# Optimization experiments

Hardware: AMD Instinct MI355X
Metric: run time of the kernel (lower is better)

## Reference

```python
import jax, jax.numpy as jnp
import numpy as np

# module config (matches init_kwargs)
SLICE_W, SLICE_H = 32, 32
STRIDE, WIDTH_INIT = 8, 8
EMBED_DIM = 512
B, H, W = 64, 32, 4096
PAD = (SLICE_W - WIDTH_INIT) // 2  # 12, width padding with constant value 1.0


def setup_inputs() -> dict:
    key = jax.random.key(0)
    k1, k2, k3, k4, k5 = jax.random.split(key, 5)
    u = lambda k, s: jax.random.uniform(k, s, jnp.float32, -0.08, 0.08)
    return {
        "images": jax.random.normal(k1, (B, 1, H, W), jnp.float32),
        "conv_w": u(k2, (1, 1, 3, 3)),          # Conv2d(1,1,3x3) weight (OIHW)
        "conv_b": u(k3, (1,)),
        "lin_w": u(k4, (SLICE_W * SLICE_H, EMBED_DIM)),  # bridge Linear, stored [in,out]
        "lin_b": u(k5, (EMBED_DIM,)),
    }


def reference(images, conv_w, conv_b, lin_w, lin_b):
    b = images.shape[0]
    # pad width with constant 1 (F.pad(..., 'constant', 1))
    padded = jnp.pad(images, ((0, 0), (0, 0), (0, 0), (PAD, PAD)), constant_values=1.0)
    # vectorized replacement of the python loop over stride positions
    starts = np.arange(0, W - 1, STRIDE)               # [S] static
    S = starts.shape[0]                                # 512
    idx = starts[:, None] + np.arange(SLICE_W)[None, :]  # [S, slice_w]
    sl = padded[:, :, :, idx]                          # [B,1,H,S,slice_w]
    sl = jnp.transpose(sl, (0, 3, 1, 2, 4))            # [B,S,1,H,slice_w]
    x = sl.reshape(b * S, 1, H, SLICE_W)               # pixels
    # embedder: Conv2d(1,1,k=3,pad=1) + ReLU
    y = jax.lax.conv_general_dilated(x, conv_w, (1, 1), ((1, 1), (1, 1)))
    y = jax.nn.relu(y + conv_b[None, :, None, None])
    # bridge: Linear(slice_w*slice_h -> embed_dim)
    flat = y.reshape(b * S, H * SLICE_W)
    out = flat @ lin_w + lin_b
    return out.reshape(b, S, EMBED_DIM)
```

## Files before the change

kernel.cpp:

```cpp
#include <hip/hip_runtime.h>
#include <cstdint>
#include <cstddef>

typedef unsigned short u16;
typedef unsigned int   u32;
typedef __attribute__((ext_vector_type(4))) float  f32x4;
typedef __attribute__((ext_vector_type(2))) u32    u32x2;
typedef __attribute__((ext_vector_type(8))) __bf16 bf16x8;

#define PSW   1056
#define ASTR  72
#define CFW   4128
#define RPAD  4128

#define WS_BT  0u
#define WS_CF  1048576u
#define WS_AB  (1048576u + 16908288u)
#define WS_NEED (1048576u + 16908288u + 4194304u)

static __device__ __forceinline__ float b2f(u32 u) {
  union { u32 i; float f; } c; c.i = u << 16; return c.f;
}
static __device__ __forceinline__ u16 f2b(float f) {
  union { float f; u32 i; } c; c.f = f;
  return (u16)((c.i + 0x7FFFu + ((c.i >> 16) & 1u)) >> 16);
}

static __device__ __forceinline__ void gl_lds16(const void* g, void* l) {
  __builtin_amdgcn_global_load_lds(
      (__attribute__((address_space(1))) unsigned int*)(void*)g,
      (__attribute__((address_space(3))) unsigned int*)l, 16, 0, 0);
}
static __device__ __forceinline__ void gl_lds4(const void* g, void* l) {
  __builtin_amdgcn_global_load_lds(
      (__attribute__((address_space(1))) unsigned int*)(void*)g,
      (__attribute__((address_space(3))) unsigned int*)l, 4, 0, 0);
}

__global__ __launch_bounds__(256) void transpose_w(const float* __restrict__ lw,
                                                   u16* __restrict__ bt) {
  __shared__ u16 tile[64][65];
  const int t  = threadIdx.x;
  const int c  = t & 63, r0 = t >> 6;
  const int n0 = blockIdx.x * 64;
  const int k0 = blockIdx.y * 64;
#pragma unroll
  for (int rr = 0; rr < 16; ++rr) {
    const int r = r0 * 16 + rr;
    tile[r][c] = f2b(lw[(size_t)(k0 + r) * 512 + n0 + c]);
  }
  __syncthreads();
#pragma unroll
  for (int rr = 0; rr < 16; ++rr) {
    const int r = r0 * 16 + rr;
    bt[(size_t)(n0 + r) * 1024 + k0 + c] = tile[c][r];
  }
}

__global__ __launch_bounds__(256) void prep(
    const float* __restrict__ img, const float* __restrict__ cw,
    const float* __restrict__ cb, u16* __restrict__ cf, u32* __restrict__ ab,
    const float* __restrict__ lw, u16* __restrict__ bt)
{
  __shared__ __align__(16) float R[3][RPAD];
  const int t = threadIdx.x;

  if (blockIdx.y == 32) {
    u16* tile = (u16*)&R[0][0];
    const int c = t & 63, r0 = t >> 6;
#pragma unroll
    for (int q = 0; q < 2; ++q) {
      const int T  = blockIdx.x * 2 + q;
      const int n0 = (T & 7) << 6, k0 = (T >> 3) << 6;
      __syncthreads();
#pragma unroll
      for (int rr = 0; rr < 16; ++rr) {
        const int r = r0 * 16 + rr;
        tile[r * 65 + c] = f2b(lw[(size_t)(k0 + r) * 512 + n0 + c]);
      }
      __syncthreads();
#pragma unroll
      for (int rr = 0; rr < 16; ++rr) {
        const int r = r0 * 16 + rr;
        bt[(size_t)(n0 + r) * 1024 + k0 + c] = tile[c * 65 + r];
      }
    }
    return;
  }

  const int b = blockIdx.x, h = blockIdx.y;
  const float* imgb = img + (size_t)b * 32 * 4096;
#pragma unroll
  for (int r = 0; r < 3; ++r) {
    const int hh = h - 1 + r;
    const int live = (hh >= 0 && hh <= 31);
    const float live1 = live ? 1.0f : 0.0f;
    const float* row = imgb + (ptrdiff_t)hh * 4096;
    for (int k = t; k < 1024; k += 256) {
      f32x4 v = (f32x4)0.0f;
      if (live) v = *(const f32x4*)(row + (k << 2));
      *(f32x4*)(&R[r][16 + (k << 2)]) = v;
    }
    if (t < 12)      R[r][4 + t]    = live1;
    else if (t < 24) R[r][4100 + t] = live1;
    else if (t < 28) R[r][4100 + t] = 0.0f;
    else if (t < 32) R[r][t - 28]   = 0.0f;
  }
  __syncthreads();
  float w[9];
#pragma unroll
  for (int q = 0; q < 9; ++q) w[q] = cw[q];
  const float bias = cb[0];
  u16* dst = cf + (size_t)(b * 32 + h) * CFW;
  if (t == 0) *(uint4*)(dst + 4120) = make_uint4(0u, 0u, 0u, 0u);

  for (int c4 = t; c4 < 1030; c4 += 256) {
    float wf[3][12];
#pragma unroll
    for (int r = 0; r < 3; ++r) {
      const f32x4* Rr = (const f32x4*)&R[r][0];
      *(f32x4*)&wf[r][0] = Rr[c4];
      *(f32x4*)&wf[r][4] = Rr[c4 + 1];
      *(f32x4*)&wf[r][8] = Rr[c4 + 2];
    }
    float o[4];
#pragma unroll
    for (int j = 0; j < 4; ++j) o[j] = bias;
#pragma unroll
    for (int r = 0; r < 3; ++r) {
      const float w0 = w[r * 3], w1 = w[r * 3 + 1], w2 = w[r * 3 + 2];
#pragma unroll
      for (int j = 0; j < 4; ++j)
        o[j] += w0 * wf[r][j + 3] + w1 * wf[r][j + 4] + w2 * wf[r][j + 5];
    }
    u32x2 pk;
    pk.x = (u32)f2b(fmaxf(o[0], 0.f)) | ((u32)f2b(fmaxf(o[1], 0.f)) << 16);
    pk.y = (u32)f2b(fmaxf(o[2], 0.f)) | ((u32)f2b(fmaxf(o[3], 0.f)) << 16);
    *(u32x2*)(dst + (c4 << 2)) = pk;
  }

  u32* abrow = ab + (size_t)(b * 32 + h) * 512;
#pragma unroll
  for (int ss = 0; ss < 2; ++ss) {
    const int s  = t + (ss << 8);
    const int X0 = (s << 3) + 4;
    float o0 = bias, o1 = bias;
#pragma unroll
    for (int r = 0; r < 3; ++r) {
      o0 += w[r * 3 + 1] * R[r][X0]      + w[r * 3 + 2] * R[r][X0 + 1];
      o1 += w[r * 3 + 0] * R[r][X0 + 30] + w[r * 3 + 1] * R[r][X0 + 31];
    }
    abrow[s] = (u32)f2b(fmaxf(o0, 0.f)) | ((u32)f2b(fmaxf(o1, 0.f)) << 16);
  }
}

__global__ __launch_bounds__(256) void gemm_k(
    const u16* __restrict__ cf, const u32* __restrict__ ab,
    const u16* __restrict__ bt, const float* __restrict__ lb,
    float* __restrict__ out)
{
  __shared__ __align__(16) char sm[4224 + 1024 + 16384];
  u16* Ps   = (u16*)sm;
  u32* Ab32 = (u32*)(sm + 4224);
  u16* Bs   = (u16*)(sm + 5248);
  float* Cs = (float*)sm;

  const int t  = threadIdx.x;
  const int orig = blockIdx.y * 4 + blockIdx.x;
  const int wg   = ((orig & 7) << 7) + (orig >> 3);
  const int nt = wg & 3, mt = wg >> 2;
  const int b  = mt >> 2, s0 = (mt & 3) << 7, n0 = nt << 7;
  const int w  = t >> 6, i = t & 63;
  const int wr = w >> 1, wc = w & 1;
  const int lq = i >> 4, lr = i & 15;

  const int cB = (i & 7) ^ ((i >> 3) & 7);
  const u16* btp = bt + (size_t)(n0 + (w << 5) + (i >> 3)) * 1024 + (cB << 3);
  u16* BsW = Bs + (w << 11);

  const int rP  = (t >= 132) ? 1 : 0;
  const int ccP = t - 132 * rP;
  const u16* cfp  = cf + (size_t)(b * 32 + rP) * CFW + (s0 << 3) + (ccP << 3);
  const u16* cfp2 = cf + (size_t)(b * 32 + 1) * CFW + (s0 << 3) + ((124 + t) << 3);
  u16* PsW = Ps + (w << 9);

  const u32* abp = ab + (size_t)(b * 32 + (t >> 7)) * 512 + s0 + (t & 127);
  u32* AbW = Ab32 + (w << 6);

  f32x4 acc[4][4];
#pragma unroll
  for (int a = 0; a < 4; ++a)
#pragma unroll
    for (int c = 0; c < 4; ++c) acc[a][c] = (f32x4)0.0f;

  for (int kk = 0; kk < 16; ++kk) {
    __syncthreads();
    gl_lds16(btp,              BsW);
    gl_lds16(btp +  8 * 1024,  BsW + 512);
    gl_lds16(btp + 16 * 1024,  BsW + 1024);
    gl_lds16(btp + 24 * 1024,  BsW + 1536);
    gl_lds16(cfp, PsW);
    if (t < 8) gl_lds16(cfp2, Ps + 2048);
    gl_lds4(abp, AbW);
    btp += 64; cfp += 2 * CFW; cfp2 += 2 * CFW; abp += 1024;
    __syncthreads();

#pragma unroll
    for (int kc = 0; kc < 2; ++kc) {
      const int bswz = (((kc << 2) + lq) ^ (lr & 7)) << 3;
      bf16x8 af[4], bfv[4];
#pragma unroll
      for (int im = 0; im < 4; ++im) {
        const int ml = wr * 64 + im * 16 + lr;
        af[im] = __builtin_bit_cast(bf16x8,
            *(const uint4*)(Ps + kc * 1056 + ((ml + lq) << 3)));
        const u32 a32 = Ab32[kc * 128 + ml];
        union { u16 u; __bf16 h; } lo, hi;
        lo.u = (u16)(a32 & 0xffffu); hi.u = (u16)(a32 >> 16);
        if (lq == 0) af[im][0] = lo.h;
        if (lq == 3) af[im][7] = hi.h;
      }
#pragma unroll
      for (int jn = 0; jn < 4; ++jn) {
        const int n = wc * 64 + jn * 16 + lr;
        bfv[jn] = __builtin_bit_cast(bf16x8, *(const uint4*)(Bs + (n << 6) + bswz));
      }
#pragma unroll
      for (int im = 0; im < 4; ++im)
#pragma unroll
        for (int jn = 0; jn < 4; ++jn)
          acc[im][jn] = __builtin_amdgcn_mfma_f32_16x16x32_bf16(
              af[im], bfv[jn], acc[im][jn], 0, 0, 0);
    }
  }

  float lbv[4];
#pragma unroll
  for (int jn = 0; jn < 4; ++jn) lbv[jn] = lb[n0 + wc * 64 + jn * 16 + lr];

  const int erow = t >> 3, ecol = (t & 7) << 4;
  const int grow_base = (mt << 7) + ((erow >> 4) * 64) + (erow & 15);

#pragma unroll
  for (int im = 0; im < 4; ++im) {
    __syncthreads();
#pragma unroll
    for (int jn = 0; jn < 4; ++jn) {
      const int cl = wc * 64 + jn * 16 + lr;
#pragma unroll
      for (int r = 0; r < 4; ++r)
        Cs[(wr * 16 + lq * 4 + r) * 132 + cl] = acc[im][jn][r] + lbv[jn];
    }
    __syncthreads();
    const size_t grow = (size_t)(grow_base + im * 16);
    float* orow = out + grow * 512 + n0 + ecol;
    const float* crow = Cs + erow * 132 + ecol;
#pragma unroll
    for (int p = 0; p < 4; ++p)
      *(f32x4*)(orow + p * 4) = *(const f32x4*)(crow + p * 4);
  }
}

__global__ __launch_bounds__(256) void fused_fallback(
    const float* __restrict__ img, const float* __restrict__ cw,
    const float* __restrict__ cb, const u16* __restrict__ bt,
    const float* __restrict__ lb, float* __restrict__ out)
{
  __shared__ __align__(16) u16 Ps[4 * PSW];
  __shared__ __align__(16) u16 As[128 * ASTR];
  __shared__ __align__(16) u16 Bs[128 * ASTR];
  const int t = threadIdx.x, nt = blockIdx.x, mt = blockIdx.y;
  const int b = mt >> 2, s0 = (mt & 3) << 7, X0 = s0 << 3, n0 = nt << 7;
  const float* imgb = img + (size_t)b * 32 * 4096;
  float cwf[9];
#pragma unroll
  for (int q = 0; q < 9; ++q) cwf[q] = cw[q];
  const float bias = cb[0];
  const int wv = t >> 6, l = t & 63;
  const int wr = wv >> 1, wc = wv & 1, lq = l >> 4, lr = l & 15;
  const int sl = t >> 1, hsel = t & 1;
  f32x4 acc[4][4];
#pragma unroll
  for (int a = 0; a < 4; ++a)
#pragma unroll
    for (int c = 0; c < 4; ++c) acc[a][c] = (f32x4)0.0f;
  for (int kk = 0; kk < 16; ++kk) {
    const int h0 = kk << 1;
    __syncthreads();
    uint4 bsv[4];
#pragma unroll
    for (int p = 0; p < 4; ++p) {
      const int idx8 = t + (p << 8);
      const int n = idx8 >> 3, k8 = idx8 & 7;
      bsv[p] = *(const uint4*)(bt + (size_t)(n0 + n) * 1024 + (kk << 6) + (k8 << 3));
    }
    for (int idx = t; idx < 4 * PSW; idx += 256) {
      const int r = idx / PSW, xi = idx - r * PSW;
      const int h = h0 - 1 + r, x = X0 - 1 + xi;
      u16 v = 0;
      if (h >= 0 && h < 32 && x >= 0 && x < 4120)
        v = (x < 12 || x >= 4108) ? (u16)0x3F80 : f2b(imgb[h * 4096 + (x - 12)]);
      Ps[idx] = v;
    }
    __syncthreads();
    {
      const int pbase = (sl << 3);
#pragma unroll
      for (int wb = 0; wb < 32; wb += 16) {
        float o[16];
#pragma unroll
        for (int j = 0; j < 16; ++j) o[j] = bias;
#pragma unroll
        for (int dr = 0; dr < 3; ++dr) {
          const u16* p = Ps + (hsel + dr) * PSW + pbase + wb;
          const uint4 va = *(const uint4*)p;
          const uint4 vb = *(const uint4*)(p + 8);
          const u32   vc = *(const u32*)(p + 16);
          float win[18];
          win[0] = b2f(va.x & 0xffffu); win[1] = b2f(va.x >> 16);
          win[2] = b2f(va.y & 0xffffu); win[3] = b2f(va.y >> 16);
          win[4] = b2f(va.z & 0xffffu); win[5] = b2f(va.z >> 16);
          win[6] = b2f(va.w & 0xffffu); win[7] = b2f(va.w >> 16);
          win[8] = b2f(vb.x & 0xffffu); win[9] = b2f(vb.x >> 16);
          win[10] = b2f(vb.y & 0xffffu); win[11] = b2f(vb.y >> 16);
          win[12] = b2f(vb.z & 0xffffu); win[13] = b2f(vb.z >> 16);
          win[14] = b2f(vb.w & 0xffffu); win[15] = b2f(vb.w >> 16);
          win[16] = b2f(vc & 0xffffu);   win[17] = b2f(vc >> 16);
          if (wb == 0) win[0] = 0.f; else win[17] = 0.f;
          const float w0 = cwf[dr * 3], w1 = cwf[dr * 3 + 1], w2 = cwf[dr * 3 + 2];
#pragma unroll
          for (int j = 0; j < 16; ++j)
            o[j] += w0 * win[j] + w1 * win[j + 1] + w2 * win[j + 2];
        }
        u32 pk[8];
#pragma unroll
        for (int q = 0; q < 8; ++q)
          pk[q] = (u32)f2b(fmaxf(o[2 * q], 0.f)) | ((u32)f2b(fmaxf(o[2 * q + 1], 0.f)) << 16);
        uint4* dst = (uint4*)(As + sl * ASTR + (hsel << 5) + wb);
        dst[0] = make_uint4(pk[0], pk[1], pk[2], pk[3]);
        dst[1] = make_uint4(pk[4], pk[5], pk[6], pk[7]);
      }
    }
#pragma unroll
    for (int p = 0; p < 4; ++p) {
      const int idx8 = t + (p << 8);
      const int n = idx8 >> 3, k8 = idx8 & 7;
      *(uint4*)(Bs + n * ASTR + (k8 << 3)) = bsv[p];
    }
    __syncthreads();
#pragma unroll
    for (int kc = 0; kc < 2; ++kc) {
      const int ko = (kc << 5) + (lq << 3);
      bf16x8 af[4], bfv[4];
#pragma unroll
      for (int im = 0; im < 4; ++im)
        af[im] = __builtin_bit_cast(bf16x8,
            *(const uint4*)(As + (wr * 64 + im * 16 + lr) * ASTR + ko));
#pragma unroll
      for (int jn = 0; jn < 4; ++jn)
        bfv[jn] = __builtin_bit_cast(bf16x8,
            *(const uint4*)(Bs + (wc * 64 + jn * 16 + lr) * ASTR + ko));
#pragma unroll
      for (int im = 0; im < 4; ++im)
#pragma unroll
        for (int jn = 0; jn < 4; ++jn)
          acc[im][jn] = __builtin_amdgcn_mfma_f32_16x16x32_bf16(
              af[im], bfv[jn], acc[im][jn], 0, 0, 0);
    }
  }
#pragma unroll
  for (int jn = 0; jn < 4; ++jn) {
    const int col = n0 + wc * 64 + jn * 16 + lr;
    const float lbv = lb[col];
#pragma unroll
    for (int im = 0; im < 4; ++im) {
      const int row0 = (mt << 7) + wr * 64 + im * 16 + (lq << 2);
#pragma unroll
      for (int r = 0; r < 4; ++r)
        out[(size_t)(row0 + r) * 512 + col] = acc[im][jn][r] + lbv;
    }
  }
}

extern "C" void kernel_launch(void* const* d_in, const int* in_sizes, int n_in,
                              void* d_out, int out_size, void* d_ws, size_t ws_size,
                              hipStream_t stream) {
  const float* img = (const float*)d_in[0];
  const float* cw  = (const float*)d_in[1];
  const float* cb  = (const float*)d_in[2];
  const float* lw  = (const float*)d_in[3];
  const float* lb  = (const float*)d_in[4];
  float* out = (float*)d_out;

  u16* btw = (u16*)((char*)d_ws + WS_BT);

  if (ws_size >= WS_NEED) {
    u16* cfp = (u16*)((char*)d_ws + WS_CF);
    u32* abp = (u32*)((char*)d_ws + WS_AB);
    prep<<<dim3(64, 33), 256, 0, stream>>>(img, cw, cb, cfp, abp, lw, btw);
    gemm_k<<<dim3(4, 256), 256, 0, stream>>>(cfp, abp, btw, lb, out);
  } else {
    transpose_w<<<dim3(8, 16), 256, 0, stream>>>(lw, btw);
    fused_fallback<<<dim3(4, 256), 256, 0, stream>>>(img, cw, cb, btw, lb, out);
  }
}
```

Measured before the change: 165.2 us.

## Double-buffer GEMM LDS stages and remap prep block indices

Splits the GEMM k-loop into stage and compute steps over two LDS buffers, so global-to-LDS loads for the next k-slice are issued while MFMAs run on the current one. This removes one barrier per iteration and hides load latency, at the cost of roughly doubling LDS use per block, which may lower occupancy. The prep kernel also moves from a 2D grid to a linearized, XCD-interleaved block-to-(b,h) mapping. It still keeps the weight-transpose blocks at h==32.

```diff
diff --git a/kernel.cpp b/kernel.cpp
--- a/kernel.cpp
+++ b/kernel.cpp
@@ -12,6 +12,7 @@
 #define ASTR  72
 #define CFW   4128
 #define RPAD  4128
+#define BUFB  21632
 
 #define WS_BT  0u
 #define WS_CF  1048576u
@@ -65,12 +66,16 @@
   __shared__ __align__(16) float R[3][RPAD];
   const int t = threadIdx.x;
 
-  if (blockIdx.y == 32) {
+  const int hwid = blockIdx.y * 64 + blockIdx.x;
+  const int g = (hwid & 7) * 264 + (hwid >> 3);
+  const int b = g / 33, h = g - b * 33;
+
+  if (h == 32) {
     u16* tile = (u16*)&R[0][0];
     const int c = t & 63, r0 = t >> 6;
 #pragma unroll
     for (int q = 0; q < 2; ++q) {
-      const int T  = blockIdx.x * 2 + q;
+      const int T  = b * 2 + q;
       const int n0 = (T & 7) << 6, k0 = (T >> 3) << 6;
       __syncthreads();
 #pragma unroll
@@ -88,7 +93,6 @@
     return;
   }
 
-  const int b = blockIdx.x, h = blockIdx.y;
   const float* imgb = img + (size_t)b * 32 * 4096;
 #pragma unroll
   for (int r = 0; r < 3; ++r) {
@@ -159,10 +163,7 @@
     const u16* __restrict__ bt, const float* __restrict__ lb,
     float* __restrict__ out)
 {
-  __shared__ __align__(16) char sm[4224 + 1024 + 16384];
-  u16* Ps   = (u16*)sm;
-  u32* Ab32 = (u32*)(sm + 4224);
-  u16* Bs   = (u16*)(sm + 5248);
+  __shared__ __align__(16) char sm[2 * BUFB];
   float* Cs = (float*)sm;
 
   const int t  = threadIdx.x;
@@ -176,16 +177,11 @@
 
   const int cB = (i & 7) ^ ((i >> 3) & 7);
   const u16* btp = bt + (size_t)(n0 + (w << 5) + (i >> 3)) * 1024 + (cB << 3);
-  u16* BsW = Bs + (w << 11);
-
   const int rP  = (t >= 132) ? 1 : 0;
   const int ccP = t - 132 * rP;
   const u16* cfp  = cf + (size_t)(b * 32 + rP) * CFW + (s0 << 3) + (ccP << 3);
   const u16* cfp2 = cf + (size_t)(b * 32 + 1) * CFW + (s0 << 3) + ((124 + t) << 3);
-  u16* PsW = Ps + (w << 9);
-
   const u32* abp = ab + (size_t)(b * 32 + (t >> 7)) * 512 + s0 + (t & 127);
-  u32* AbW = Ab32 + (w << 6);
 
   f32x4 acc[4][4];
 #pragma unroll
@@ -193,18 +189,24 @@
 #pragma unroll
     for (int c = 0; c < 4; ++c) acc[a][c] = (f32x4)0.0f;
 
-  for (int kk = 0; kk < 16; ++kk) {
-    __syncthreads();
+  auto STAGE = [&](char* base) {
+    u16* PsB = (u16*)base;
+    u32* AbB = (u32*)(base + 4224);
+    u16* BsW = (u16*)(base + 5248) + (w << 11);
     gl_lds16(btp,              BsW);
     gl_lds16(btp +  8 * 1024,  BsW + 512);
     gl_lds16(btp + 16 * 1024,  BsW + 1024);
     gl_lds16(btp + 24 * 1024,  BsW + 1536);
-    gl_lds16(cfp, PsW);
-    if (t < 8) gl_lds16(cfp2, Ps + 2048);
-    gl_lds4(abp, AbW);
+    gl_lds16(cfp, PsB + (w << 9));
+    if (t < 8) gl_lds16(cfp2, PsB + 2048);
+    gl_lds4(abp, AbB + (w << 6));
     btp += 64; cfp += 2 * CFW; cfp2 += 2 * CFW; abp += 1024;
-    __syncthreads();
-
+  };
+
+  auto COMPUTE = [&](const char* base) {
+    const u16* PsC = (const u16*)base;
+    const u32* AbC = (const u32*)(base + 4224);
+    const u16* BsC = (const u16*)(base + 5248);
 #pragma unroll
     for (int kc = 0; kc < 2; ++kc) {
       const int bswz = (((kc << 2) + lq) ^ (lr & 7)) << 3;
@@ -213,8 +215,8 @@
       for (int im = 0; im < 4; ++im) {
         const int ml = wr * 64 + im * 16 + lr;
         af[im] = __builtin_bit_cast(bf16x8,
-            *(const uint4*)(Ps + kc * 1056 + ((ml + lq) << 3)));
-        const u32 a32 = Ab32[kc * 128 + ml];
+            *(const uint4*)(PsC + kc * 1056 + ((ml + lq) << 3)));
+        const u32 a32 = AbC[kc * 128 + ml];
         union { u16 u; __bf16 h; } lo, hi;
         lo.u = (u16)(a32 & 0xffffu); hi.u = (u16)(a32 >> 16);
         if (lq == 0) af[im][0] = lo.h;
@@ -223,7 +225,7 @@
 #pragma unroll
       for (int jn = 0; jn < 4; ++jn) {
         const int n = wc * 64 + jn * 16 + lr;
-        bfv[jn] = __builtin_bit_cast(bf16x8, *(const uint4*)(Bs + (n << 6) + bswz));
+        bfv[jn] = __builtin_bit_cast(bf16x8, *(const uint4*)(BsC + (n << 6) + bswz));
       }
 #pragma unroll
       for (int im = 0; im < 4; ++im)
@@ -232,7 +234,23 @@
           acc[im][jn] = __builtin_amdgcn_mfma_f32_16x16x32_bf16(
               af[im], bfv[jn], acc[im][jn], 0, 0, 0);
     }
-  }
+  };
+
+  STAGE(sm);
+  __syncthreads();
+#pragma unroll 1
+  for (int kk = 0; kk < 14; kk += 2) {
+    STAGE(sm + BUFB);
+    COMPUTE(sm);
+    __syncthreads();
+    STAGE(sm);
+    COMPUTE(sm + BUFB);
+    __syncthreads();
+  }
+  STAGE(sm + BUFB);
+  COMPUTE(sm);
+  __syncthreads();
+  COMPUTE(sm + BUFB);
 
   float lbv[4];
 #pragma unroll
```

After: 164.4 us. No clear change (-0.5%).

## Restructure conv prep into row-streaming blocks with async LDS ring buffer

Applied to the files above, without the earlier changes.

Replaces the per-(batch,row) prep kernel, which loaded three image rows for every output row, with blocks that each handle a half-width column chunk and eight consecutive rows. Rows are streamed into a 4-slot LDS ring with global_load_lds, so each input row is loaded once per block and the next row's load overlaps with the current row's convolution. Block size goes to 512 threads and the weight-transpose work is packed into 8 blocks. The price is more synchronisation per row, tricky boundary indexing for the split halves and edge columns, and fewer, larger blocks.

```diff
diff --git a/kernel.cpp b/kernel.cpp
--- a/kernel.cpp
+++ b/kernel.cpp
@@ -5,13 +5,14 @@
 typedef unsigned short u16;
 typedef unsigned int   u32;
 typedef __attribute__((ext_vector_type(4))) float  f32x4;
+typedef __attribute__((ext_vector_type(2))) float  f32x2;
 typedef __attribute__((ext_vector_type(2))) u32    u32x2;
 typedef __attribute__((ext_vector_type(8))) __bf16 bf16x8;
 
 #define PSW   1056
 #define ASTR  72
 #define CFW   4128
-#define RPAD  4128
+#define WIN   2080
 
 #define WS_BT  0u
 #define WS_CF  1048576u
@@ -57,100 +58,139 @@
   }
 }
 
-__global__ __launch_bounds__(256) void prep(
+__global__ __launch_bounds__(512) void prep2(
     const float* __restrict__ img, const float* __restrict__ cw,
     const float* __restrict__ cb, u16* __restrict__ cf, u32* __restrict__ ab,
     const float* __restrict__ lw, u16* __restrict__ bt)
 {
-  __shared__ __align__(16) float R[3][RPAD];
-  const int t = threadIdx.x;
-
-  if (blockIdx.y == 32) {
-    u16* tile = (u16*)&R[0][0];
+  __shared__ __align__(16) float RING[4 * WIN];
+  const int t  = threadIdx.x;
+  const int id = blockIdx.x;
+
+  if (id >= 512) {
+    u16* tile = (u16*)&RING[0];
     const int c = t & 63, r0 = t >> 6;
-#pragma unroll
-    for (int q = 0; q < 2; ++q) {
-      const int T  = blockIdx.x * 2 + q;
+    for (int q = 0; q < 16; ++q) {
+      const int T  = (id - 512) * 16 + q;
       const int n0 = (T & 7) << 6, k0 = (T >> 3) << 6;
       __syncthreads();
 #pragma unroll
-      for (int rr = 0; rr < 16; ++rr) {
-        const int r = r0 * 16 + rr;
+      for (int rr = 0; rr < 8; ++rr) {
+        const int r = r0 * 8 + rr;
         tile[r * 65 + c] = f2b(lw[(size_t)(k0 + r) * 512 + n0 + c]);
       }
       __syncthreads();
 #pragma unroll
-      for (int rr = 0; rr < 16; ++rr) {
-        const int r = r0 * 16 + rr;
+      for (int rr = 0; rr < 8; ++rr) {
+        const int r = r0 * 8 + rr;
         bt[(size_t)(n0 + r) * 1024 + k0 + c] = tile[c * 65 + r];
       }
     }
     return;
   }
 
-  const int b = blockIdx.x, h = blockIdx.y;
+  const int b  = id >> 3, sub = id & 7;
+  const int ch = sub & 1, hq = sub >> 1;
+  const int h0 = hq << 3;
+  const int col0   = ch ? 2032 : 0;
+  const int wstart = ch ? 0 : 16;
   const float* imgb = img + (size_t)b * 32 * 4096;
-#pragma unroll
-  for (int r = 0; r < 3; ++r) {
-    const int hh = h - 1 + r;
-    const int live = (hh >= 0 && hh <= 31);
-    const float live1 = live ? 1.0f : 0.0f;
-    const float* row = imgb + (ptrdiff_t)hh * 4096;
-    for (int k = t; k < 1024; k += 256) {
-      f32x4 v = (f32x4)0.0f;
-      if (live) v = *(const f32x4*)(row + (k << 2));
-      *(f32x4*)(&R[r][16 + (k << 2)]) = v;
-    }
-    if (t < 12)      R[r][4 + t]    = live1;
-    else if (t < 24) R[r][4100 + t] = live1;
-    else if (t < 28) R[r][4100 + t] = 0.0f;
-    else if (t < 32) R[r][t - 28]   = 0.0f;
-  }
+
+  float w9[9];
+#pragma unroll
+  for (int q = 0; q < 9; ++q) w9[q] = cw[q];
+  const float bias = cb[0];
+
+  auto STAGE = [&](int i) {
+    float* sp = RING + (i & 3) * WIN;
+    const int hh = h0 - 1 + i;
+    if (hh >= 0 && hh <= 31) {
+      const float* src = imgb + (ptrdiff_t)hh * 4096 + col0;
+      gl_lds16(src + 4 * t, sp + wstart + ((t >> 6) << 8));
+      if (t < 4) gl_lds16(src + 2048 + 4 * t, sp + wstart + 2048);
+      if (ch == 0) { if (t < 16) sp[t] = (t < 4) ? 0.0f : 1.0f; }
+      else         { if (t < 16) sp[2064 + t] = (t < 12) ? 1.0f : 0.0f; }
+    } else {
+      *(f32x4*)(sp + (t << 2)) = (f32x4)0.0f;
+      if (t < 8) *(f32x4*)(sp + 2048 + (t << 2)) = (f32x4)0.0f;
+    }
+  };
+
+  STAGE(0); STAGE(1); STAGE(2);
   __syncthreads();
-  float w[9];
-#pragma unroll
-  for (int q = 0; q < 9; ++q) w[q] = cw[q];
-  const float bias = cb[0];
-  u16* dst = cf + (size_t)(b * 32 + h) * CFW;
-  if (t == 0) *(uint4*)(dst + 4120) = make_uint4(0u, 0u, 0u, 0u);
-
-  for (int c4 = t; c4 < 1030; c4 += 256) {
-    float wf[3][12];
-#pragma unroll
-    for (int r = 0; r < 3; ++r) {
-      const f32x4* Rr = (const f32x4*)&R[r][0];
-      *(f32x4*)&wf[r][0] = Rr[c4];
-      *(f32x4*)&wf[r][4] = Rr[c4 + 1];
-      *(f32x4*)&wf[r][8] = Rr[c4 + 2];
-    }
-    float o[4];
-#pragma unroll
-    for (int j = 0; j < 4; ++j) o[j] = bias;
-#pragma unroll
-    for (int r = 0; r < 3; ++r) {
-      const float w0 = w[r * 3], w1 = w[r * 3 + 1], w2 = w[r * 3 + 2];
-#pragma unroll
-      for (int j = 0; j < 4; ++j)
-        o[j] += w0 * wf[r][j + 3] + w1 * wf[r][j + 4] + w2 * wf[r][j + 5];
-    }
-    u32x2 pk;
-    pk.x = (u32)f2b(fmaxf(o[0], 0.f)) | ((u32)f2b(fmaxf(o[1], 0.f)) << 16);
-    pk.y = (u32)f2b(fmaxf(o[2], 0.f)) | ((u32)f2b(fmaxf(o[3], 0.f)) << 16);
-    *(u32x2*)(dst + (c4 << 2)) = pk;
-  }
-
-  u32* abrow = ab + (size_t)(b * 32 + h) * 512;
-#pragma unroll
-  for (int ss = 0; ss < 2; ++ss) {
-    const int s  = t + (ss << 8);
-    const int X0 = (s << 3) + 4;
-    float o0 = bias, o1 = bias;
-#pragma unroll
-    for (int r = 0; r < 3; ++r) {
-      o0 += w[r * 3 + 1] * R[r][X0]      + w[r * 3 + 2] * R[r][X0 + 1];
-      o1 += w[r * 3 + 0] * R[r][X0 + 30] + w[r * 3 + 1] * R[r][X0 + 31];
-    }
-    abrow[s] = (u32)f2b(fmaxf(o0, 0.f)) | ((u32)f2b(fmaxf(o1, 0.f)) << 16);
+
+#pragma unroll 1
+  for (int it = 0; it < 8; ++it) {
+    if (it < 7) STAGE(3 + it);
+    const int h = h0 + it;
+    const float* R0 = RING + (( it      ) & 3) * WIN;
+    const float* R1 = RING + ((it + 1) & 3) * WIN;
+    const float* R2 = RING + ((it + 2) & 3) * WIN;
+    u16* cfrow = cf + (size_t)(b * 32 + h) * CFW;
+
+    f32x4 aa0, aa1, aa2;
+    auto CONV4 = [&](int tl, bool exp) {
+      const int w4 = tl << 2;
+      const f32x4 a0 = *(const f32x4*)(R0 + w4), b0 = *(const f32x4*)(R0 + w4 + 4);
+      const float c0 = R0[w4 + 8];
+      const f32x4 a1 = *(const f32x4*)(R1 + w4), b1 = *(const f32x4*)(R1 + w4 + 4);
+      const float c1 = R1[w4 + 8];
+      const f32x4 a2 = *(const f32x4*)(R2 + w4), b2 = *(const f32x4*)(R2 + w4 + 4);
+      const float c2 = R2[w4 + 8];
+      float o0 = bias, o1 = bias, o2 = bias, o3 = bias;
+      o0 += w9[0] * a0.w + w9[1] * b0.x + w9[2] * b0.y;
+      o1 += w9[0] * b0.x + w9[1] * b0.y + w9[2] * b0.z;
+      o2 += w9[0] * b0.y + w9[1] * b0.z + w9[2] * b0.w;
+      o3 += w9[0] * b0.z + w9[1] * b0.w + w9[2] * c0;
+      o0 += w9[3] * a1.w + w9[4] * b1.x + w9[5] * b1.y;
+      o1 += w9[3] * b1.x + w9[4] * b1.y + w9[5] * b1.z;
+      o2 += w9[3] * b1.y + w9[4] * b1.z + w9[5] * b1.w;
+      o3 += w9[3] * b1.z + w9[4] * b1.w + w9[5] * c1;
+      o0 += w9[6] * a2.w + w9[7] * b2.x + w9[8] * b2.y;
+      o1 += w9[6] * b2.x + w9[7] * b2.y + w9[8] * b2.z;
+      o2 += w9[6] * b2.y + w9[7] * b2.z + w9[8] * b2.w;
+      o3 += w9[6] * b2.z + w9[7] * b2.w + w9[8] * c2;
+      u32x2 pk;
+      pk.x = (u32)f2b(fmaxf(o0, 0.f)) | ((u32)f2b(fmaxf(o1, 0.f)) << 16);
+      pk.y = (u32)f2b(fmaxf(o2, 0.f)) | ((u32)f2b(fmaxf(o3, 0.f)) << 16);
+      *(u32x2*)(cfrow + (ch << 11) + (tl << 2)) = pk;
+      if (exp) { aa0 = a0; aa1 = a1; aa2 = a2; }
+    };
+
+    CONV4(t, true);
+    if (ch == 1) {
+      if (t < 6) CONV4(512 + t, false);
+      if (t == 0) { u32x2 z; z.x = 0u; z.y = 0u; *(u32x2*)(cfrow + 4120) = z; }
+    }
+
+    u16* abh = (u16*)ab + (size_t)(b * 32 + h) * 1024;
+    if (t & 1) {
+      const int j = t >> 1;
+      float v = bias;
+      v += w9[1] * aa0.x + w9[2] * aa0.y;
+      v += w9[4] * aa1.x + w9[5] * aa1.y;
+      v += w9[7] * aa2.x + w9[8] * aa2.y;
+      abh[((ch << 8) + j) << 1] = f2b(fmaxf(v, 0.f));
+    } else if (t >= 8) {
+      const int j = (t - 8) >> 1;
+      float v = bias;
+      v += w9[0] * aa0.z + w9[1] * aa0.w;
+      v += w9[3] * aa1.z + w9[4] * aa1.w;
+      v += w9[6] * aa2.z + w9[7] * aa2.w;
+      abh[(((ch << 8) + j) << 1) | 1] = f2b(fmaxf(v, 0.f));
+    } else {
+      const int j = 252 + (t >> 1);
+      const int wq = 8 * j + 34;
+      const f32x2 u0 = *(const f32x2*)(R0 + wq);
+      const f32x2 u1 = *(const f32x2*)(R1 + wq);
+      const f32x2 u2 = *(const f32x2*)(R2 + wq);
+      float v = bias;
+      v += w9[0] * u0.x + w9[1] * u0.y;
+      v += w9[3] * u1.x + w9[4] * u1.y;
+      v += w9[6] * u2.x + w9[7] * u2.y;
+      abh[(((ch << 8) + j) << 1) | 1] = f2b(fmaxf(v, 0.f));
+    }
+    __syncthreads();
   }
 }
 
@@ -397,7 +437,7 @@
   if (ws_size >= WS_NEED) {
     u16* cfp = (u16*)((char*)d_ws + WS_CF);
     u32* abp = (u32*)((char*)d_ws + WS_AB);
-    prep<<<dim3(64, 33), 256, 0, stream>>>(img, cw, cb, cfp, abp, lw, btw);
+    prep2<<<dim3(520), 512, 0, stream>>>(img, cw, cb, cfp, abp, lw, btw);
     gemm_k<<<dim3(4, 256), 256, 0, stream>>>(cfp, abp, btw, lb, out);
   } else {
     transpose_w<<<dim3(8, 16), 256, 0, stream>>>(lw, btw);
```

Result: faster. 161.8 us (-2.0%).
